# Optimization experiments

Measured on AMD Instinct MI355X. Metric: run time of the kernel, lower is better.

## Reference

```python
import jax, jax.numpy as jnp
import numpy as np

THETA = 10.0      # neuron['theta']
TAU_SR = 10.0     # neuron['tauSr']
TAU_REF = 1.0     # neuron['tauRef']
SCALE_REF = 2.0   # neuron['scaleRef']
TAU_RHO = 1.0     # neuron['tauRho']
SCALE_RHO = 1.0   # neuron['scaleRho']
EPS = 0.01        # kernel truncation epsilon
TS = 1.0          # simulation['Ts']
T_SAMPLE = 256    # time steps == seq_len (forward sets tSample = embed_out.size(1))


def _alpha_kernel(tau, mult):
    # slayerPytorch _calculateAlphaKernel: mult * t/tau * exp(1 - t/tau), truncated
    ker = []
    for t in np.arange(0.0, T_SAMPLE * TS, TS):
        v = mult * t / tau * np.exp(1.0 - t / tau)
        if abs(v) < EPS and t > tau:
            break
        ker.append(v)
    return np.asarray(ker, dtype=np.float32)


def psp(x, srm_kernel):
    # Causal temporal filter: out[t] = Ts * sum_k srm[k] * x[t-k];  x: (B, C, T)
    B, C, T = x.shape
    K = srm_kernel.shape[0]
    lhs = x.reshape(B * C, 1, T)
    rhs = srm_kernel[::-1].reshape(1, 1, K)  # reverse: correlation -> convolution
    out = jax.lax.conv_general_dilated(lhs, rhs, (1,), [(K - 1, 0)])
    return out.reshape(B, C, T) * TS


def _spike_scan(u, ref_kernel):
    # Sequential threshold with refractory feedback (SLAYER getSpikes). u: (B, C, T)
    B, C, T = u.shape
    future = ref_kernel[1:]  # ref_kernel[0] == 0, so spike at t only affects t+1..
    R = future.shape[0]

    def step(r, u_t):
        m = u_t + r[..., 0]                       # membrane incl. past refractory
        s = (m >= THETA).astype(u.dtype)
        r = jnp.concatenate([r[..., 1:], jnp.zeros_like(r[..., :1])], axis=-1)
        r = r + s[..., None] * future             # schedule refractory response
        return r, (s, m)

    r0 = jnp.zeros((B, C, R), u.dtype)
    _, (s, m) = jax.lax.scan(step, r0, jnp.moveaxis(u, -1, 0))
    return jnp.moveaxis(s, 0, -1), jnp.moveaxis(m, 0, -1)


@jax.custom_vjp
def spike(u, ref_kernel):
    return _spike_scan(u, ref_kernel)[0]


def _spike_fwd(u, ref_kernel):
    s, m = _spike_scan(u, ref_kernel)
    return s, (m, ref_kernel)


def _spike_bwd(res, g):
    # SLAYER surrogate gradient: straight-through pdf on post-refractory membrane
    m, ref_kernel = res
    tau = TAU_RHO * THETA
    pdf = (SCALE_RHO / tau) * jnp.exp(-jnp.abs(m - THETA) / tau)
    return g * pdf, jnp.zeros_like(ref_kernel)


spike.defvjp(_spike_fwd, _spike_bwd)


def setup_inputs() -> dict:
    key = jax.random.key(0)
    k1, k2, k3, k4 = jax.random.split(key, 4)
    VOCAB, EMB, HID, OUT, B = 50000, 300, 512, 10, 64
    feed_data = jax.random.randint(k1, (B, T_SAMPLE), 0, VOCAB)
    emb_weight = jax.random.normal(k2, (VOCAB, EMB), jnp.float32)
    W1 = jax.random.normal(k3, (HID, EMB), jnp.float32) * (4.0 / np.sqrt(EMB))
    W2 = jax.random.normal(k4, (OUT, HID), jnp.float32) * (4.0 / np.sqrt(HID))
    return {
        "feed_data": feed_data,
        "emb_weight": emb_weight,
        "W1": W1,
        "W2": W2,
        "srm_kernel": jnp.asarray(_alpha_kernel(TAU_SR, 1.0)),
        "ref_kernel": jnp.asarray(_alpha_kernel(TAU_REF, -SCALE_REF * THETA)),
    }


def reference(feed_data, emb_weight, W1, W2, srm_kernel, ref_kernel):
    x = emb_weight[feed_data]                 # (B, T, E); dropout = identity (eval)
    x = jnp.transpose(x, (0, 2, 1))           # (B, E, T) -- transpose(1,2)
    h = jnp.einsum('he,bet->bht', W1, x)      # slayer.dense == 1x1x1 conv3d, no bias
    h = spike(psp(h, srm_kernel), ref_kernel)
    o = jnp.einsum('oh,bht->bot', W2, h)
    return spike(psp(o, srm_kernel), ref_kernel)  # (B, OUT, T)
```

## Files before the change

kernel.cpp:

```cpp
#include <hip/hip_runtime.h>

#define BB    64
#define TT    256
#define EMBD  300
#define HIDD  512
#define OUTC  10
#define THETA 10.0
#define FUTN  12
#define KSMAX 80
#define XSTR  260
#define WSTR  34
#define HSTR  257
#define CTILE 32

__global__ __launch_bounds__(256)
void w2cvt_kernel(const float* __restrict__ W2, double* __restrict__ w2d)
{
    const int k = blockIdx.x * 256 + threadIdx.x;
    if (k < OUTC * HIDD) w2d[k] = (double)W2[k];
}

__global__ __launch_bounds__(256, 3)
void gemm1_kernel(const int* __restrict__ feed, const float* __restrict__ emb,
                  const float* __restrict__ W1, double* __restrict__ m1,
                  int cbase, int chn)
{
    __shared__ float  xs[16 * XSTR];
    __shared__ double wl[16 * WSTR];
    __shared__ int    idxb[TT];

    const int tid = threadIdx.x;
    const int c0l = blockIdx.x * CTILE;
    const int c0  = cbase + c0l;
    const int b   = blockIdx.y;

    idxb[tid] = feed[b * TT + tid];
    __syncthreads();

    const int cg = tid >> 6, tg = tid & 63;
    const int es = tid & 15, ts = tid >> 4;

    int myidx[16];
#pragma unroll
    for (int k = 0; k < 16; ++k) myidx[k] = idxb[ts + 16 * k];

    double acc[4][8];
#pragma unroll
    for (int i = 0; i < 4; ++i)
#pragma unroll
        for (int j = 0; j < 8; ++j) acc[i][j] = 0.0;

    const int NCH = (EMBD + 15) / 16;
    for (int ch = 0; ch < NCH; ++ch) {
        const int e0 = ch * 16;
        const int ec = min(16, EMBD - e0);
        if (es < ec) {
#pragma unroll
            for (int k = 0; k < 16; ++k) {
                const int t = ts + 16 * k;
                xs[es * XSTR + t] = emb[(size_t)myidx[k] * EMBD + e0 + es];
            }
        }
        {
            int u = tid;
#pragma unroll
            for (int rep = 0; rep < 2; ++rep) {
                const int c = u >> 4, e = u & 15;
                if (e < ec)
                    wl[e * WSTR + c] = (double)W1[(size_t)(c0 + c) * EMBD + e0 + e];
                u += 256;
            }
        }
        __syncthreads();
        for (int e = 0; e < ec; ++e) {
            const float4  xv = *(const float4*)&xs[e * XSTR + 4 * tg];
            const double* wp = &wl[e * WSTR + 8 * cg];
            const double2 w01 = *(const double2*)(wp + 0);
            const double2 w23 = *(const double2*)(wp + 2);
            const double2 w45 = *(const double2*)(wp + 4);
            const double2 w67 = *(const double2*)(wp + 6);
            const double wv[8] = { w01.x, w01.y, w23.x, w23.y,
                                   w45.x, w45.y, w67.x, w67.y };
            const double xd[4] = { (double)xv.x, (double)xv.y,
                                   (double)xv.z, (double)xv.w };
#pragma unroll
            for (int i = 0; i < 4; ++i)
#pragma unroll
                for (int j = 0; j < 8; ++j)
                    acc[i][j] = fma(xd[i], wv[j], acc[i][j]);
        }
        __syncthreads();
    }

#pragma unroll
    for (int j = 0; j < 8; ++j) {
        double* dst = &m1[((size_t)b * chn + c0l + 8 * cg + j) * TT + 4 * tg];
        *(double2*)(dst + 0) = make_double2(acc[0][j], acc[1][j]);
        *(double2*)(dst + 2) = make_double2(acc[2][j], acc[3][j]);
    }
}

__global__ __launch_bounds__(256)
void firscan_kernel(const double* __restrict__ m1, const float* __restrict__ srm,
                    const float* __restrict__ refk, unsigned char* __restrict__ s1,
                    int Ks, int Kr, int cbase, int chn)
{
    __shared__ double        h[16 * HSTR];
    __shared__ unsigned char sb[16 * 260];
    __shared__ double        srm_sm[KSMAX];

    const int tid = threadIdx.x;
    const int c0l = blockIdx.x * 16;
    const int b   = blockIdx.y;

    if (tid < KSMAX) srm_sm[tid] = (tid < Ks) ? (double)srm[tid] : 0.0;

    for (int u = tid; u < 16 * TT; u += 256)
        h[(u >> 8) * HSTR + (u & 255)] =
            m1[((size_t)b * chn + c0l + (u >> 8)) * TT + (u & 255)];
    __syncthreads();

    const int cf = tid & 15, tb = tid >> 4;
    const double* hrow = &h[cf * HSTR];
    double pout[16];
#pragma unroll
    for (int k = 0; k < 16; ++k) pout[k] = 0.0;
#pragma unroll
    for (int pp = 0; pp < 2; ++pp) {
        const int t0 = tb * 16 + pp * 8;
        double win[8];
#pragma unroll
        for (int k = 0; k < 8; ++k) win[k] = hrow[t0 + k];
        for (int jb = 0; jb < KSMAX; jb += 8) {
#pragma unroll
            for (int jj = 0; jj < 8; ++jj) {
                const double sj = srm_sm[jb + jj];
#pragma unroll
                for (int i = 0; i < 8; ++i)
                    pout[pp * 8 + i] = fma(win[(8 + i - jj) & 7], sj, pout[pp * 8 + i]);
                const int idx = t0 - (jb + jj) - 1;
                win[(7 - jj) & 7] = (idx >= 0) ? hrow[idx] : 0.0;
            }
        }
    }
    __syncthreads();
#pragma unroll
    for (int k = 0; k < 16; ++k)
        h[cf * HSTR + tb * 16 + k] = pout[k];
    __syncthreads();

    if (tid < 16) {
        double fut[FUTN], rsh[FUTN];
#pragma unroll
        for (int i = 0; i < FUTN; ++i) {
            fut[i] = (i + 1 < Kr) ? (double)refk[i + 1] : 0.0;
            rsh[i] = 0.0;
        }
        const double*  hr = &h[tid * HSTR];
        unsigned char* sr = &sb[tid * 260];
        for (int t = 0; t < TT; ++t) {
            const double m  = hr[t] + rsh[0];
            const double sv = (m >= THETA) ? 1.0 : 0.0;
#pragma unroll
            for (int i = 0; i < FUTN - 1; ++i) rsh[i] = fma(sv, fut[i], rsh[i + 1]);
            rsh[FUTN - 1] = sv * fut[FUTN - 1];
            sr[t] = (unsigned char)(sv != 0.0 ? 1 : 0);
        }
    }
    __syncthreads();

    {
        const int tl2 = tid & 63;
#pragma unroll
        for (int r = 0; r < 4; ++r) {
            const int c = (tid >> 6) + 4 * r;
            const unsigned int v = *(const unsigned int*)&sb[c * 260 + 4 * tl2];
            *(unsigned int*)&s1[((size_t)b * HIDD + cbase + c0l + c) * TT + 4 * tl2] = v;
        }
    }
}

__global__ __launch_bounds__(256, 2)
void layer2a_kernel(const unsigned char* __restrict__ s1,
                    const double* __restrict__ w2d, double* __restrict__ m2)
{
    __shared__ double w2l[OUTC * HIDD];
    __shared__ double red[4][OUTC][65];

    const int tid = threadIdx.x;
    const int b = blockIdx.x, q = blockIdx.y;
    const int tl = tid & 63, hq = tid >> 6;
    const int t  = q * 64 + tl;

    for (int u = tid; u < OUTC * HIDD; u += 256) w2l[u] = w2d[u];
    __syncthreads();

    double p[OUTC];
#pragma unroll
    for (int oc = 0; oc < OUTC; ++oc) p[oc] = 0.0;

    const unsigned char* sp = s1 + ((size_t)b * HIDD + hq * 128) * TT + t;
    for (int h0 = 0; h0 < 128; ++h0) {
        const double sv = (double)sp[(size_t)h0 * TT];
        const int h = hq * 128 + h0;
#pragma unroll
        for (int oc = 0; oc < OUTC; ++oc)
            p[oc] = fma(sv, w2l[oc * HIDD + h], p[oc]);
    }
#pragma unroll
    for (int oc = 0; oc < OUTC; ++oc) red[hq][oc][tl] = p[oc];
    __syncthreads();

    for (int u = tid; u < OUTC * 64; u += 256) {
        const int oc = u >> 6, t2 = u & 63;
        const double s = ((red[0][oc][t2] + red[1][oc][t2]) +
                          red[2][oc][t2]) + red[3][oc][t2];
        m2[((size_t)b * OUTC + oc) * TT + q * 64 + t2] = s;
    }
}

__global__ __launch_bounds__(256)
void layer2b_kernel(const double* __restrict__ m2, const float* __restrict__ srm,
                    const float* __restrict__ refk, float* __restrict__ out,
                    int Ks, int Kr)
{
    __shared__ double mh[OUTC][257];
    __shared__ double uh[OUTC][257];
    __shared__ double srm_sm[KSMAX];
    __shared__ unsigned char s2[OUTC][260];

    const int tid = threadIdx.x;
    const int b   = blockIdx.x;

    if (tid < KSMAX) srm_sm[tid] = (tid < Ks) ? (double)srm[tid] : 0.0;
    for (int u = tid; u < OUTC * TT; u += 256)
        mh[u >> 8][u & 255] = m2[(size_t)b * OUTC * TT + u];
    __syncthreads();

    double p[OUTC];
#pragma unroll
    for (int oc = 0; oc < OUTC; ++oc) p[oc] = 0.0;
    for (int j = 0; j < KSMAX; ++j) {
        const int idx = tid - j;
        if (idx >= 0) {
            const double sj = srm_sm[j];
#pragma unroll
            for (int oc = 0; oc < OUTC; ++oc)
                p[oc] = fma(mh[oc][idx], sj, p[oc]);
        }
    }
#pragma unroll
    for (int oc = 0; oc < OUTC; ++oc) uh[oc][tid] = p[oc];
    __syncthreads();

    if (tid < OUTC) {
        double fut[FUTN], rsh[FUTN];
#pragma unroll
        for (int i = 0; i < FUTN; ++i) {
            fut[i] = (i + 1 < Kr) ? (double)refk[i + 1] : 0.0;
            rsh[i] = 0.0;
        }
        for (int t = 0; t < TT; ++t) {
            const double m  = uh[tid][t] + rsh[0];
            const double sv = (m >= THETA) ? 1.0 : 0.0;
#pragma unroll
            for (int i = 0; i < FUTN - 1; ++i) rsh[i] = fma(sv, fut[i], rsh[i + 1]);
            rsh[FUTN - 1] = sv * fut[FUTN - 1];
            s2[tid][t] = (unsigned char)(sv != 0.0 ? 1 : 0);
        }
    }
    __syncthreads();

    for (int u = tid; u < OUTC * TT; u += 256)
        out[(size_t)b * OUTC * TT + u] = (float)s2[u >> 8][u & 255];
}

extern "C" void kernel_launch(void* const* d_in, const int* in_sizes, int n_in,
                              void* d_out, int out_size, void* d_ws, size_t ws_size,
                              hipStream_t stream)
{
    const int*   feed = (const int*)  d_in[0];
    const float* emb  = (const float*)d_in[1];
    const float* W1   = (const float*)d_in[2];
    const float* W2   = (const float*)d_in[3];
    const float* srm  = (const float*)d_in[4];
    const float* refk = (const float*)d_in[5];
    const int Ks = in_sizes[4];
    const int Kr = in_sizes[5];

    const size_t S1B  = (size_t)BB * HIDD * TT;
    const size_t W2DB = (size_t)OUTC * HIDD * 8;
    const size_t M2B  = (size_t)BB * OUTC * TT * 8;
    unsigned char* s1c = (unsigned char*)d_ws;
    double* w2d = (double*)((char*)d_ws + S1B);
    double* m2  = (double*)((char*)d_ws + S1B + W2DB);
    double* m1  = (double*)((char*)d_ws + S1B + W2DB + M2B);
    const size_t fixed = S1B + W2DB + M2B;
    const size_t avail = (ws_size > fixed) ? ws_size - fixed : 0;

    int chn = 32;
    if ((size_t)BB * 512 * TT * 8 <= avail) chn = 512;
    else if ((size_t)BB * 256 * TT * 8 <= avail) chn = 256;
    else if ((size_t)BB * 128 * TT * 8 <= avail) chn = 128;
    else if ((size_t)BB *  64 * TT * 8 <= avail) chn = 64;

    float* out = (float*)d_out;

    w2cvt_kernel<<<dim3(20), 256, 0, stream>>>(W2, w2d);
    for (int cb = 0; cb < HIDD; cb += chn) {
        gemm1_kernel  <<<dim3(chn / CTILE, BB), 256, 0, stream>>>(
            feed, emb, W1, m1, cb, chn);
        firscan_kernel<<<dim3(chn / 16, BB),    256, 0, stream>>>(
            m1, srm, refk, s1c, Ks, Kr, cb, chn);
    }
    layer2a_kernel<<<dim3(BB, 4), 256, 0, stream>>>(s1c, w2d, m2);
    layer2b_kernel<<<dim3(BB),    256, 0, stream>>>(m2, srm, refk, out, Ks, Kr);
}
```

Before: 439.6 us.

## Retile layer-1 GEMM over time with all channels per block, time-major m1

The first-layer GEMM now tiles over 32 time steps with all 512 hidden channels per 512-thread block. Each embedding row is gathered once per block instead of once per channel tile, and W1 is streamed as float4 rows into a padded double layout. m1 becomes time-major (B,T,H), and the FIR/scan kernel is reworked for 32 channels per block with a transposed shared tile and prefetch in the serial scan. The workspace chunking fallback is removed, which assumes the workspace always holds the full fp64 m1 buffer. W1 is now re-read by every time tile.

```diff
diff --git a/kernel.cpp b/kernel.cpp
--- a/kernel.cpp
+++ b/kernel.cpp
@@ -8,10 +8,11 @@
 #define THETA 10.0
 #define FUTN  12
 #define KSMAX 80
-#define XSTR  260
-#define WSTR  34
-#define HSTR  257
-#define CTILE 32
+#define GT    32
+#define GE    8
+#define WGRP  9
+#define WROW  (64 * WGRP)
+#define HSTR  33
 
 __global__ __launch_bounds__(256)
 void w2cvt_kernel(const float* __restrict__ W2, double* __restrict__ w2d)
@@ -20,29 +21,23 @@
     if (k < OUTC * HIDD) w2d[k] = (double)W2[k];
 }
 
-__global__ __launch_bounds__(256, 3)
+__global__ __launch_bounds__(512)
 void gemm1_kernel(const int* __restrict__ feed, const float* __restrict__ emb,
-                  const float* __restrict__ W1, double* __restrict__ m1,
-                  int cbase, int chn)
-{
-    __shared__ float  xs[16 * XSTR];
-    __shared__ double wl[16 * WSTR];
-    __shared__ int    idxb[TT];
+                  const float* __restrict__ W1, double* __restrict__ m1)
+{
+    __shared__ double wl[GE * WROW];
+    __shared__ double xs[GE][GT + 1];
+    __shared__ int    idxb[GT];
 
     const int tid = threadIdx.x;
-    const int c0l = blockIdx.x * CTILE;
-    const int c0  = cbase + c0l;
+    const int t0  = blockIdx.x * GT;
     const int b   = blockIdx.y;
 
-    idxb[tid] = feed[b * TT + tid];
-    __syncthreads();
-
-    const int cg = tid >> 6, tg = tid & 63;
-    const int es = tid & 15, ts = tid >> 4;
-
-    int myidx[16];
-#pragma unroll
-    for (int k = 0; k < 16; ++k) myidx[k] = idxb[ts + 16 * k];
+    if (tid < GT) idxb[tid] = feed[b * TT + t0 + tid];
+    __syncthreads();
+
+    const int cg = tid & 63;
+    const int tg = tid >> 6;
 
     double acc[4][8];
 #pragma unroll
@@ -50,87 +45,104 @@
 #pragma unroll
         for (int j = 0; j < 8; ++j) acc[i][j] = 0.0;
 
-    const int NCH = (EMBD + 15) / 16;
+    const int NCH = (EMBD + GE - 1) / GE;
     for (int ch = 0; ch < NCH; ++ch) {
-        const int e0 = ch * 16;
-        const int ec = min(16, EMBD - e0);
-        if (es < ec) {
-#pragma unroll
-            for (int k = 0; k < 16; ++k) {
-                const int t = ts + 16 * k;
-                xs[es * XSTR + t] = emb[(size_t)myidx[k] * EMBD + e0 + es];
-            }
-        }
+        const int e0 = ch * GE;
         {
-            int u = tid;
-#pragma unroll
-            for (int rep = 0; rep < 2; ++rep) {
-                const int c = u >> 4, e = u & 15;
-                if (e < ec)
-                    wl[e * WSTR + c] = (double)W1[(size_t)(c0 + c) * EMBD + e0 + e];
-                u += 256;
-            }
+            const int c = tid;
+            float4 wa = make_float4(0.f, 0.f, 0.f, 0.f);
+            float4 wb = make_float4(0.f, 0.f, 0.f, 0.f);
+            if (e0 < EMBD)     wa = *(const float4*)&W1[(size_t)c * EMBD + e0];
+            if (e0 + 4 < EMBD) wb = *(const float4*)&W1[(size_t)c * EMBD + e0 + 4];
+            const int g = (c >> 3) * WGRP + (c & 7);
+            wl[0 * WROW + g] = (double)wa.x;
+            wl[1 * WROW + g] = (double)wa.y;
+            wl[2 * WROW + g] = (double)wa.z;
+            wl[3 * WROW + g] = (double)wa.w;
+            wl[4 * WROW + g] = (double)wb.x;
+            wl[5 * WROW + g] = (double)wb.y;
+            wl[6 * WROW + g] = (double)wb.z;
+            wl[7 * WROW + g] = (double)wb.w;
+        }
+        if (tid < 256) {
+            const int t = tid >> 3, e = tid & 7;
+            const float v = (e0 + e < EMBD)
+                ? emb[(size_t)idxb[t] * EMBD + e0 + e] : 0.f;
+            xs[e][t] = (double)v;
         }
         __syncthreads();
-        for (int e = 0; e < ec; ++e) {
-            const float4  xv = *(const float4*)&xs[e * XSTR + 4 * tg];
-            const double* wp = &wl[e * WSTR + 8 * cg];
-            const double2 w01 = *(const double2*)(wp + 0);
-            const double2 w23 = *(const double2*)(wp + 2);
-            const double2 w45 = *(const double2*)(wp + 4);
-            const double2 w67 = *(const double2*)(wp + 6);
-            const double wv[8] = { w01.x, w01.y, w23.x, w23.y,
-                                   w45.x, w45.y, w67.x, w67.y };
-            const double xd[4] = { (double)xv.x, (double)xv.y,
-                                   (double)xv.z, (double)xv.w };
-#pragma unroll
-            for (int i = 0; i < 4; ++i)
-#pragma unroll
-                for (int j = 0; j < 8; ++j)
-                    acc[i][j] = fma(xd[i], wv[j], acc[i][j]);
+
+#pragma unroll
+        for (int e = 0; e < GE; ++e) {
+            const double* wp = &wl[e * WROW + cg * WGRP];
+            const double w0 = wp[0], w1 = wp[1], w2 = wp[2], w3 = wp[3];
+            const double w4 = wp[4], w5 = wp[5], w6 = wp[6], w7 = wp[7];
+            const double x0 = xs[e][4 * tg + 0];
+            const double x1 = xs[e][4 * tg + 1];
+            const double x2 = xs[e][4 * tg + 2];
+            const double x3 = xs[e][4 * tg + 3];
+            acc[0][0] = fma(x0, w0, acc[0][0]); acc[0][1] = fma(x0, w1, acc[0][1]);
+            acc[0][2] = fma(x0, w2, acc[0][2]); acc[0][3] = fma(x0, w3, acc[0][3]);
+            acc[0][4] = fma(x0, w4, acc[0][4]); acc[0][5] = fma(x0, w5, acc[0][5]);
+            acc[0][6] = fma(x0, w6, acc[0][6]); acc[0][7] = fma(x0, w7, acc[0][7]);
+            acc[1][0] = fma(x1, w0, acc[1][0]); acc[1][1] = fma(x1, w1, acc[1][1]);
+            acc[1][2] = fma(x1, w2, acc[1][2]); acc[1][3] = fma(x1, w3, acc[1][3]);
+            acc[1][4] = fma(x1, w4, acc[1][4]); acc[1][5] = fma(x1, w5, acc[1][5]);
+            acc[1][6] = fma(x1, w6, acc[1][6]); acc[1][7] = fma(x1, w7, acc[1][7]);
+            acc[2][0] = fma(x2, w0, acc[2][0]); acc[2][1] = fma(x2, w1, acc[2][1]);
+            acc[2][2] = fma(x2, w2, acc[2][2]); acc[2][3] = fma(x2, w3, acc[2][3]);
+            acc[2][4] = fma(x2, w4, acc[2][4]); acc[2][5] = fma(x2, w5, acc[2][5]);
+            acc[2][6] = fma(x2, w6, acc[2][6]); acc[2][7] = fma(x2, w7, acc[2][7]);
+            acc[3][0] = fma(x3, w0, acc[3][0]); acc[3][1] = fma(x3, w1, acc[3][1]);
+            acc[3][2] = fma(x3, w2, acc[3][2]); acc[3][3] = fma(x3, w3, acc[3][3]);
+            acc[3][4] = fma(x3, w4, acc[3][4]); acc[3][5] = fma(x3, w5, acc[3][5]);
+            acc[3][6] = fma(x3, w6, acc[3][6]); acc[3][7] = fma(x3, w7, acc[3][7]);
         }
         __syncthreads();
     }
 
 #pragma unroll
-    for (int j = 0; j < 8; ++j) {
-        double* dst = &m1[((size_t)b * chn + c0l + 8 * cg + j) * TT + 4 * tg];
-        *(double2*)(dst + 0) = make_double2(acc[0][j], acc[1][j]);
-        *(double2*)(dst + 2) = make_double2(acc[2][j], acc[3][j]);
-    }
-}
-
-__global__ __launch_bounds__(256)
+    for (int i = 0; i < 4; ++i) {
+        double* dst = &m1[((size_t)b * TT + t0 + 4 * tg + i) * HIDD + 8 * cg];
+        *(double2*)(dst + 0) = make_double2(acc[i][0], acc[i][1]);
+        *(double2*)(dst + 2) = make_double2(acc[i][2], acc[i][3]);
+        *(double2*)(dst + 4) = make_double2(acc[i][4], acc[i][5]);
+        *(double2*)(dst + 6) = make_double2(acc[i][6], acc[i][7]);
+    }
+}
+
+__global__ __launch_bounds__(512)
 void firscan_kernel(const double* __restrict__ m1, const float* __restrict__ srm,
                     const float* __restrict__ refk, unsigned char* __restrict__ s1,
-                    int Ks, int Kr, int cbase, int chn)
-{
-    __shared__ double        h[16 * HSTR];
-    __shared__ unsigned char sb[16 * 260];
+                    int Ks, int Kr)
+{
+    __shared__ double        h[TT * HSTR];
+    __shared__ unsigned char sb[32 * 260];
     __shared__ double        srm_sm[KSMAX];
 
     const int tid = threadIdx.x;
-    const int c0l = blockIdx.x * 16;
+    const int c0  = blockIdx.x * 32;
     const int b   = blockIdx.y;
 
     if (tid < KSMAX) srm_sm[tid] = (tid < Ks) ? (double)srm[tid] : 0.0;
 
-    for (int u = tid; u < 16 * TT; u += 256)
-        h[(u >> 8) * HSTR + (u & 255)] =
-            m1[((size_t)b * chn + c0l + (u >> 8)) * TT + (u & 255)];
-    __syncthreads();
-
-    const int cf = tid & 15, tb = tid >> 4;
-    const double* hrow = &h[cf * HSTR];
+    for (int u = tid; u < TT * 32; u += 512) {
+        const int t = u >> 5, c = u & 31;
+        h[t * HSTR + c] = m1[((size_t)b * TT + t) * HIDD + c0 + c];
+    }
+    __syncthreads();
+
+    const int c  = tid & 31, tb = tid >> 5;
+    const int tf = tb * 16;
     double pout[16];
 #pragma unroll
     for (int k = 0; k < 16; ++k) pout[k] = 0.0;
 #pragma unroll
     for (int pp = 0; pp < 2; ++pp) {
-        const int t0 = tb * 16 + pp * 8;
+        const int tq = tf + pp * 8;
         double win[8];
 #pragma unroll
-        for (int k = 0; k < 8; ++k) win[k] = hrow[t0 + k];
+        for (int k = 0; k < 8; ++k) win[k] = h[(tq + k) * HSTR + c];
         for (int jb = 0; jb < KSMAX; jb += 8) {
 #pragma unroll
             for (int jj = 0; jj < 8; ++jj) {
@@ -138,28 +150,30 @@
 #pragma unroll
                 for (int i = 0; i < 8; ++i)
                     pout[pp * 8 + i] = fma(win[(8 + i - jj) & 7], sj, pout[pp * 8 + i]);
-                const int idx = t0 - (jb + jj) - 1;
-                win[(7 - jj) & 7] = (idx >= 0) ? hrow[idx] : 0.0;
+                const int idx = tq - (jb + jj) - 1;
+                win[(7 - jj) & 7] = (idx >= 0) ? h[idx * HSTR + c] : 0.0;
             }
         }
     }
     __syncthreads();
 #pragma unroll
     for (int k = 0; k < 16; ++k)
-        h[cf * HSTR + tb * 16 + k] = pout[k];
-    __syncthreads();
-
-    if (tid < 16) {
+        h[(tf + k) * HSTR + c] = pout[k];
+    __syncthreads();
+
+    if (tid < 32) {
         double fut[FUTN], rsh[FUTN];
 #pragma unroll
         for (int i = 0; i < FUTN; ++i) {
             fut[i] = (i + 1 < Kr) ? (double)refk[i + 1] : 0.0;
             rsh[i] = 0.0;
         }
-        const double*  hr = &h[tid * HSTR];
         unsigned char* sr = &sb[tid * 260];
+        double un = h[0 * HSTR + tid];
         for (int t = 0; t < TT; ++t) {
-            const double m  = hr[t] + rsh[0];
+            const double uc = un;
+            un = (t < TT - 1) ? h[(t + 1) * HSTR + tid] : 0.0;
+            const double m  = uc + rsh[0];
             const double sv = (m >= THETA) ? 1.0 : 0.0;
 #pragma unroll
             for (int i = 0; i < FUTN - 1; ++i) rsh[i] = fma(sv, fut[i], rsh[i + 1]);
@@ -169,14 +183,10 @@
     }
     __syncthreads();
 
-    {
-        const int tl2 = tid & 63;
-#pragma unroll
-        for (int r = 0; r < 4; ++r) {
-            const int c = (tid >> 6) + 4 * r;
-            const unsigned int v = *(const unsigned int*)&sb[c * 260 + 4 * tl2];
-            *(unsigned int*)&s1[((size_t)b * HIDD + cbase + c0l + c) * TT + 4 * tl2] = v;
-        }
+    for (int u = tid; u < 32 * (TT / 4); u += 512) {
+        const int cc = u >> 6, tw = u & 63;
+        const unsigned int v = *(const unsigned int*)&sb[cc * 260 + 4 * tw];
+        *(unsigned int*)&s1[((size_t)b * HIDD + c0 + cc) * TT + 4 * tw] = v;
     }
 }
 
@@ -202,10 +212,10 @@
     const unsigned char* sp = s1 + ((size_t)b * HIDD + hq * 128) * TT + t;
     for (int h0 = 0; h0 < 128; ++h0) {
         const double sv = (double)sp[(size_t)h0 * TT];
-        const int h = hq * 128 + h0;
+        const int hh = hq * 128 + h0;
 #pragma unroll
         for (int oc = 0; oc < OUTC; ++oc)
-            p[oc] = fma(sv, w2l[oc * HIDD + h], p[oc]);
+            p[oc] = fma(sv, w2l[oc * HIDD + hh], p[oc]);
     }
 #pragma unroll
     for (int oc = 0; oc < OUTC; ++oc) red[hq][oc][tl] = p[oc];
@@ -295,24 +305,11 @@
     double* w2d = (double*)((char*)d_ws + S1B);
     double* m2  = (double*)((char*)d_ws + S1B + W2DB);
     double* m1  = (double*)((char*)d_ws + S1B + W2DB + M2B);
-    const size_t fixed = S1B + W2DB + M2B;
-    const size_t avail = (ws_size > fixed) ? ws_size - fixed : 0;
-
-    int chn = 32;
-    if ((size_t)BB * 512 * TT * 8 <= avail) chn = 512;
-    else if ((size_t)BB * 256 * TT * 8 <= avail) chn = 256;
-    else if ((size_t)BB * 128 * TT * 8 <= avail) chn = 128;
-    else if ((size_t)BB *  64 * TT * 8 <= avail) chn = 64;
-
-    float* out = (float*)d_out;
-
-    w2cvt_kernel<<<dim3(20), 256, 0, stream>>>(W2, w2d);
-    for (int cb = 0; cb < HIDD; cb += chn) {
-        gemm1_kernel  <<<dim3(chn / CTILE, BB), 256, 0, stream>>>(
-            feed, emb, W1, m1, cb, chn);
-        firscan_kernel<<<dim3(chn / 16, BB),    256, 0, stream>>>(
-            m1, srm, refk, s1c, Ks, Kr, cb, chn);
-    }
-    layer2a_kernel<<<dim3(BB, 4), 256, 0, stream>>>(s1c, w2d, m2);
-    layer2b_kernel<<<dim3(BB),    256, 0, stream>>>(m2, srm, refk, out, Ks, Kr);
-}
+    float*  out = (float*)d_out;
+
+    w2cvt_kernel  <<<dim3(20),           256, 0, stream>>>(W2, w2d);
+    gemm1_kernel  <<<dim3(TT / GT, BB),  512, 0, stream>>>(feed, emb, W1, m1);
+    firscan_kernel<<<dim3(HIDD / 32, BB),512, 0, stream>>>(m1, srm, refk, s1c, Ks, Kr);
+    layer2a_kernel<<<dim3(BB, 4),        256, 0, stream>>>(s1c, w2d, m2);
+    layer2b_kernel<<<dim3(BB),           256, 0, stream>>>(m2, srm, refk, out, Ks, Kr);
+}
```

New measurement: 562.9 us. +28.0%, slower.
